# Performance work log

Hardware: AMD Instinct MI355X
Metric: run time of the kernel (lower is better)

Reference implementation:

```python
import jax, jax.numpy as jnp
import numpy as np

B, H, W, DIM, HEADS = 4, 32, 32, 768, 12
HD = DIM // HEADS


def setup_inputs() -> dict:
    key = jax.random.key(0)
    ks = jax.random.split(key, 5)
    return {
        "x": jax.random.normal(ks[0], (B, H, W, DIM), jnp.float32),
        "qkv_w": jax.random.normal(ks[1], (3 * DIM, DIM), jnp.float32) * 0.02,
        "qkv_b": jnp.zeros((3 * DIM,), jnp.float32),
        "proj_w": jax.random.normal(ks[2], (DIM, DIM), jnp.float32) * 0.02,
        "proj_b": jnp.zeros((DIM,), jnp.float32),
        "rel_pos_h": jax.random.normal(ks[3], (2 * H - 1, HD), jnp.float32) * 0.02,
        "rel_pos_w": jax.random.normal(ks[4], (2 * W - 1, HD), jnp.float32) * 0.02,
    }


def reference(x, qkv_w, qkv_b, proj_w, proj_b, rel_pos_h, rel_pos_w):
    b, h, w, dim = x.shape
    heads = HEADS
    hd = dim // heads
    n = h * w
    scale = hd ** -0.5

    xf = x.reshape(b, n, dim)
    qkv = xf @ qkv_w.T + qkv_b                          # [b, n, 3*dim]
    qkv = qkv.reshape(b, n, 3, heads, hd)
    qkv = jnp.transpose(qkv, (2, 0, 3, 1, 4)).reshape(3, b * heads, n, hd)
    q, k, v = qkv[0], qkv[1], qkv[2]                    # [b*heads, n, hd]

    # decomposed relative position bias (q_size == k_size, no interpolation)
    idx_h = jnp.arange(h)[:, None] - jnp.arange(h)[None, :] + (h - 1)
    idx_w = jnp.arange(w)[:, None] - jnp.arange(w)[None, :] + (w - 1)
    Rh = rel_pos_h[idx_h]                               # [h, h, hd]
    Rw = rel_pos_w[idx_w]                               # [w, w, hd]
    r_q = q.reshape(b * heads, h, w, hd)
    rel_h = jnp.einsum('bhwc,hkc->bhwk', r_q, Rh)       # [bH, h, w, h]
    rel_w = jnp.einsum('bhwc,wkc->bhwk', r_q, Rw)       # [bH, h, w, w]
    bias = (rel_h[:, :, :, :, None] + rel_w[:, :, :, None, :]).reshape(b * heads, n, n)

    attn = jax.nn.softmax(jnp.einsum('bnd,bmd->bnm', q * scale, k) + bias, axis=-1)
    out = jnp.einsum('bnm,bmd->bnd', attn, v)           # [b*heads, n, hd]
    out = out.reshape(b, heads, n, hd).transpose(0, 2, 1, 3).reshape(b, n, dim)
    out = out @ proj_w.T + proj_b
    return out.reshape(b, h, w, dim)
```

## Files before the change

kernel.cpp:

```cpp
#include <hip/hip_runtime.h>

#define DEV_INLINE static __device__ __forceinline__

typedef __attribute__((ext_vector_type(8))) short bf16x8;
typedef __attribute__((ext_vector_type(4))) float f32x4;
typedef __attribute__((ext_vector_type(16))) float f32x16;

DEV_INLINE unsigned short f2bf(float f) {
  union { float f; unsigned int u; } v; v.f = f;
  unsigned int u = v.u;
  u += 0x7FFFu + ((u >> 16) & 1u);
  return (unsigned short)(u >> 16);
}
DEV_INLINE float bf2f(unsigned short h) {
  union { unsigned int u; float f; } v; v.u = ((unsigned int)h) << 16; return v.f;
}

__global__ __launch_bounds__(256) void cvt_f32_bf16(const float* __restrict__ in,
                                                    unsigned short* __restrict__ out, int n4) {
  int i = blockIdx.x * 256 + threadIdx.x;
  if (i >= n4) return;
  float4 v = reinterpret_cast<const float4*>(in)[i];
  ushort4 o;
  o.x = f2bf(v.x); o.y = f2bf(v.y); o.z = f2bf(v.z); o.w = f2bf(v.w);
  reinterpret_cast<ushort4*>(out)[i] = o;
}

template <int MODE>
__global__ __launch_bounds__(256) void gemm_bf16(const unsigned short* __restrict__ A,
                                                 const unsigned short* __restrict__ Bw,
                                                 const float* __restrict__ bias,
                                                 float* __restrict__ outF,
                                                 unsigned short* __restrict__ qo,
                                                 unsigned short* __restrict__ ko,
                                                 unsigned short* __restrict__ vo) {
  __shared__ unsigned short As[2][128 * 32];
  __shared__ unsigned short Bs[2][128 * 32];

  const int tid = threadIdx.x;
  const int lane = tid & 63;
  const int wv = tid >> 6;
  const int wrow = (wv >> 1) * 64;
  const int wcol = (wv & 1) * 64;
  const int m0 = blockIdx.y * 128;
  const int n0 = blockIdx.x * 128;
  const int l15 = lane & 15;
  const int lg = lane >> 4;

  const int srow = lane >> 2;
  const int seg  = (lane & 3) ^ (srow & 3);

  f32x4 acc[4][4];
#pragma unroll
  for (int i = 0; i < 4; ++i)
#pragma unroll
    for (int j = 0; j < 4; ++j) acc[i][j] = (f32x4){0.f, 0.f, 0.f, 0.f};

#define GSTAGE(KT, B)                                                                        \
  do {                                                                                       \
    _Pragma("unroll") for (int pp = 0; pp < 2; ++pp) {                                       \
      int p = wv * 2 + pp;                                   \
      int row = p * 16 + srow;                                                               \
      const unsigned short* ga = &A[(m0 + row) * 768 + (KT) * 32 + seg * 8];                 \
      __builtin_amdgcn_global_load_lds(                                                      \
          (const __attribute__((address_space(1))) unsigned int*)ga,                         \
          (__attribute__((address_space(3))) unsigned int*)&As[B][p * 512], 16, 0, 0);       \
      const unsigned short* gb = &Bw[(n0 + row) * 768 + (KT) * 32 + seg * 8];                \
      __builtin_amdgcn_global_load_lds(                                                      \
          (const __attribute__((address_space(1))) unsigned int*)gb,                         \
          (__attribute__((address_space(3))) unsigned int*)&Bs[B][p * 512], 16, 0, 0);       \
    }                                                                                        \
  } while (0)

  GSTAGE(0, 0);

  for (int kt = 0; kt < 24; ++kt) {
    const int b = kt & 1;
    __syncthreads();
    if (kt < 23) GSTAGE(kt + 1, b ^ 1);

    const int soff = (lg ^ (l15 & 3)) * 8;
    bf16x8 aF[4], bF[4];
#pragma unroll
    for (int i = 0; i < 4; ++i)
      aF[i] = *reinterpret_cast<const bf16x8*>(&As[b][(wrow + i * 16 + l15) * 32 + soff]);
#pragma unroll
    for (int j = 0; j < 4; ++j)
      bF[j] = *reinterpret_cast<const bf16x8*>(&Bs[b][(wcol + j * 16 + l15) * 32 + soff]);
#pragma unroll
    for (int i = 0; i < 4; ++i)
#pragma unroll
      for (int j = 0; j < 4; ++j)
        acc[i][j] = __builtin_amdgcn_mfma_f32_16x16x32_bf16(aF[i], bF[j], acc[i][j], 0, 0, 0);
  }
#undef GSTAGE

#pragma unroll
  for (int i = 0; i < 4; ++i) {
#pragma unroll
    for (int j = 0; j < 4; ++j) {
#pragma unroll
      for (int r = 0; r < 4; ++r) {
        int row = m0 + wrow + i * 16 + (lane >> 4) * 4 + r;
        int col = n0 + wcol + j * 16 + l15;
        float val = acc[i][j][r] + bias[col];
        if (MODE == 0) {
          int t = col / 768;
          int rem = col - t * 768;
          int head = rem >> 6;
          int c = rem & 63;
          int bb = row >> 10;
          int n = row & 1023;
          if (t == 0) val *= 1.44269504f;
          if (t == 1) val *= 0.125f;
          unsigned short* dst = (t == 0) ? qo : (t == 1) ? ko : vo;
          dst[((bb * 12 + head) * 1024 + n) * 64 + c] = f2bf(val);
        } else {
          outF[row * 768 + col] = val;
        }
      }
    }
  }
}

__global__ __launch_bounds__(256) void vtrans(const unsigned short* __restrict__ vb,
                                              unsigned short* __restrict__ vt) {
  __shared__ unsigned short t[64][72];
  const int n0 = blockIdx.x * 64;
  const int bh = blockIdx.y;
  const int tid = threadIdx.x;
#pragma unroll
  for (int i = 0; i < 4; ++i) {
    int s = tid + i * 256;
    int row = s >> 4, c4 = (s & 15) * 4;
    *reinterpret_cast<ushort4*>(&t[row][c4]) =
        *reinterpret_cast<const ushort4*>(&vb[(bh * 1024 + n0 + row) * 64 + c4]);
  }
  __syncthreads();
#pragma unroll
  for (int i = 0; i < 4; ++i) {
    int s = tid + i * 256;
    int d = s >> 4, n4 = (s & 15) * 4;
    ushort4 o;
    o.x = t[n4 + 0][d]; o.y = t[n4 + 1][d]; o.z = t[n4 + 2][d]; o.w = t[n4 + 3][d];
    *reinterpret_cast<ushort4*>(&vt[(bh * 64 + d) * 1024 + n0 + n4]) = o;
  }
}

DEV_INLINE f32x4 mfma16(bf16x8 a, bf16x8 b, f32x4 c) {
  return __builtin_amdgcn_mfma_f32_16x16x32_bf16(a, b, c, 0, 0, 0);
}

__global__ __launch_bounds__(64) void rel_mfma16(const unsigned short* __restrict__ q,
                                                 const float* __restrict__ rph,
                                                 const float* __restrict__ rpw,
                                                 unsigned short* __restrict__ relwb,
                                                 float* __restrict__ relh) {
  __shared__ unsigned short qs[32 * 72];
  __shared__ unsigned short rhh[32 * 72], rhl[32 * 72];
  __shared__ unsigned short rwh[64 * 72], rwl[64 * 72];
  __shared__ float relh_s[32 * 36];
  __shared__ unsigned short relw_s[32 * 40];

  const int lane = threadIdx.x;
  const int l15 = lane & 15;
  const int lg = lane >> 4;
  const int qh = blockIdx.x;
  const int bh = blockIdx.y;

#pragma unroll
  for (int it = 0; it < 4; ++it) {
    int s = lane + it * 64;
    int row = s >> 3, ch = s & 7;
    *reinterpret_cast<int4*>(&qs[row * 72 + ch * 8]) =
        *reinterpret_cast<const int4*>(&q[(bh * 1024 + qh * 32 + row) * 64 + ch * 8]);
  }
#pragma unroll
  for (int it = 0; it < 8; ++it) {
    int s = lane + it * 64;
    int row = s >> 4, c4 = (s & 15) * 4;
    float4 v = *reinterpret_cast<const float4*>(&rph[(qh + row) * 64 + c4]);
    ushort4 h, l;
    h.x = f2bf(v.x); l.x = f2bf(v.x - bf2f(h.x));
    h.y = f2bf(v.y); l.y = f2bf(v.y - bf2f(h.y));
    h.z = f2bf(v.z); l.z = f2bf(v.z - bf2f(h.z));
    h.w = f2bf(v.w); l.w = f2bf(v.w - bf2f(h.w));
    *reinterpret_cast<ushort4*>(&rhh[row * 72 + c4]) = h;
    *reinterpret_cast<ushort4*>(&rhl[row * 72 + c4]) = l;
  }
#pragma unroll
  for (int it = 0; it < 16; ++it) {
    int s = lane + it * 64;
    int row = s >> 4, c4 = (s & 15) * 4;
    float4 v = (float4){0.f, 0.f, 0.f, 0.f};
    if (row < 63) v = *reinterpret_cast<const float4*>(&rpw[row * 64 + c4]);
    ushort4 h, l;
    h.x = f2bf(v.x); l.x = f2bf(v.x - bf2f(h.x));
    h.y = f2bf(v.y); l.y = f2bf(v.y - bf2f(h.y));
    h.z = f2bf(v.z); l.z = f2bf(v.z - bf2f(h.z));
    h.w = f2bf(v.w); l.w = f2bf(v.w - bf2f(h.w));
    *reinterpret_cast<ushort4*>(&rwh[row * 72 + c4]) = h;
    *reinterpret_cast<ushort4*>(&rwl[row * 72 + c4]) = l;
  }
  __syncthreads();

  const int k0 = lg * 8, k1 = 32 + lg * 8;
  bf16x8 fq[2][2], fhh[2][2], fhl[2][2], fwh[4][2], fwl[4][2];
#pragma unroll
  for (int t = 0; t < 2; ++t) {
    fq[t][0]  = *reinterpret_cast<const bf16x8*>(&qs[(t * 16 + l15) * 72 + k0]);
    fq[t][1]  = *reinterpret_cast<const bf16x8*>(&qs[(t * 16 + l15) * 72 + k1]);
    fhh[t][0] = *reinterpret_cast<const bf16x8*>(&rhh[(t * 16 + l15) * 72 + k0]);
    fhh[t][1] = *reinterpret_cast<const bf16x8*>(&rhh[(t * 16 + l15) * 72 + k1]);
    fhl[t][0] = *reinterpret_cast<const bf16x8*>(&rhl[(t * 16 + l15) * 72 + k0]);
    fhl[t][1] = *reinterpret_cast<const bf16x8*>(&rhl[(t * 16 + l15) * 72 + k1]);
  }
#pragma unroll
  for (int t = 0; t < 4; ++t) {
    fwh[t][0] = *reinterpret_cast<const bf16x8*>(&rwh[(t * 16 + l15) * 72 + k0]);
    fwh[t][1] = *reinterpret_cast<const bf16x8*>(&rwh[(t * 16 + l15) * 72 + k1]);
    fwl[t][0] = *reinterpret_cast<const bf16x8*>(&rwl[(t * 16 + l15) * 72 + k0]);
    fwl[t][1] = *reinterpret_cast<const bf16x8*>(&rwl[(t * 16 + l15) * 72 + k1]);
  }

  f32x4 ah[2][2];
#pragma unroll
  for (int i = 0; i < 2; ++i)
#pragma unroll
    for (int jj = 0; jj < 2; ++jj) {
      f32x4 a = (f32x4){0.f, 0.f, 0.f, 0.f};
      a = mfma16(fhh[i][0], fq[jj][0], a);
      a = mfma16(fhh[i][1], fq[jj][1], a);
      a = mfma16(fhl[i][0], fq[jj][0], a);
      a = mfma16(fhl[i][1], fq[jj][1], a);
      ah[i][jj] = a;
    }
  f32x4 aw[2][4];
#pragma unroll
  for (int i = 0; i < 2; ++i)
#pragma unroll
    for (int jj = 0; jj < 4; ++jj) {
      f32x4 a = (f32x4){0.f, 0.f, 0.f, 0.f};
      a = mfma16(fq[i][0], fwh[jj][0], a);
      a = mfma16(fq[i][1], fwh[jj][1], a);
      a = mfma16(fq[i][0], fwl[jj][0], a);
      a = mfma16(fq[i][1], fwl[jj][1], a);
      aw[i][jj] = a;
    }

#pragma unroll
  for (int i = 0; i < 2; ++i)
#pragma unroll
    for (int jj = 0; jj < 2; ++jj)
#pragma unroll
      for (int r = 0; r < 4; ++r) {
        int t = i * 16 + lg * 4 + r;
        int qw = jj * 16 + l15;
        relh_s[qw * 36 + 31 - t] = ah[i][jj][r];
      }
#pragma unroll
  for (int i = 0; i < 2; ++i)
#pragma unroll
    for (int jj = 0; jj < 4; ++jj)
#pragma unroll
      for (int r = 0; r < 4; ++r) {
        int qw = i * 16 + lg * 4 + r;
        int d = jj * 16 + l15;
        int kw = qw + 31 - d;
        if (kw >= 0 && kw < 32) relw_s[qw * 40 + kw] = f2bf(aw[i][jj][r]);
      }
  __syncthreads();

#pragma unroll
  for (int it = 0; it < 4; ++it) {
    int s = lane + it * 64;
    int row = s >> 3, c4 = (s & 7) * 4;
    *reinterpret_cast<float4*>(&relh[(bh * 1024 + qh * 32 + row) * 32 + c4]) =
        *reinterpret_cast<const float4*>(&relh_s[row * 36 + c4]);
  }
#pragma unroll
  for (int it = 0; it < 2; ++it) {
    int s = lane + it * 64;
    int row = s >> 2, ch = s & 3;
    *reinterpret_cast<int4*>(&relwb[(bh * 1024 + qh * 32 + row) * 32 + ch * 8]) =
        *reinterpret_cast<const int4*>(&relw_s[row * 40 + ch * 8]);
  }
}

DEV_INLINE f32x16 mfma32(bf16x8 a, bf16x8 b, f32x16 c) {
  return __builtin_amdgcn_mfma_f32_32x32x16_bf16(a, b, c, 0, 0, 0);
}

DEV_INLINE bf16x8 make_pa(const float* p) {
  unsigned int W0, W1, W2, W3;
  asm("v_cvt_pk_bf16_f32 %0, %1, %2" : "=v"(W0) : "v"(p[0]), "v"(p[1]));
  asm("v_cvt_pk_bf16_f32 %0, %1, %2" : "=v"(W1) : "v"(p[2]), "v"(p[3]));
  asm("v_cvt_pk_bf16_f32 %0, %1, %2" : "=v"(W2) : "v"(p[4]), "v"(p[5]));
  asm("v_cvt_pk_bf16_f32 %0, %1, %2" : "=v"(W3) : "v"(p[6]), "v"(p[7]));
  asm("v_permlane32_swap_b32 %0, %1" : "+v"(W0), "+v"(W2));
  asm("v_permlane32_swap_b32 %0, %1" : "+v"(W1), "+v"(W3));
  union { unsigned int w[4]; bf16x8 v; } u;
  u.w[0] = W0; u.w[1] = W1; u.w[2] = W2; u.w[3] = W3;
  return u.v;
}

__global__ __launch_bounds__(128) void attn2(const unsigned short* __restrict__ kg,
                                             const unsigned short* __restrict__ vtg,
                                             const unsigned short* __restrict__ qg,
                                             const unsigned short* __restrict__ relwb,
                                             const float* __restrict__ relh,
                                             unsigned short* __restrict__ ao) {
  __shared__ unsigned short k_lin[2][64 * 64];
  __shared__ unsigned short v_lin[2][64 * 64];

  const int tid = threadIdx.x;
  const int lane = tid & 63;
  const int wv = tid >> 6;
  const int l31 = lane & 31;
  const int hi = lane >> 5;

  const int bid = blockIdx.x;
  const int swz = (bid & 7) * 96 + (bid >> 3);
  const int bh = swz >> 4;
  const int qt = swz & 15;
  const int q0 = qt * 64 + wv * 32;

  bf16x8 qf[6];
  {
    const unsigned short* qrow = &qg[(bh * 1024 + q0 + l31) * 64 + hi * 8];
#pragma unroll
    for (int c = 0; c < 4; ++c)
      qf[c] = *reinterpret_cast<const bf16x8*>(&qrow[c * 16]);
    const unsigned short* wrow = &relwb[(bh * 1024 + q0 + l31) * 32 + hi * 8];
    qf[4] = *reinterpret_cast<const bf16x8*>(&wrow[0]);
    qf[5] = *reinterpret_cast<const bf16x8*>(&wrow[16]);
  }

  bf16x8 ohf0, ohf1;
  {
    int t0 = l31 - 8 * hi;
    int t1 = l31 - 16 - 8 * hi;
    union { unsigned int w[4]; bf16x8 v; } u0, u1;
#pragma unroll
    for (int w = 0; w < 4; ++w) {
      u0.w[w] = (t0 >= 0 && (t0 >> 1) == w) ? ((t0 & 1) ? 0x3F800000u : 0x3F80u) : 0u;
      u1.w[w] = (t1 >= 0 && (t1 >> 1) == w) ? ((t1 & 1) ? 0x3F800000u : 0x3F80u) : 0u;
    }
    ohf0 = u0.v; ohf1 = u1.v;
  }

  f32x16 O0, O1;
#pragma unroll
  for (int r = 0; r < 16; ++r) { O0[r] = 0.f; O1[r] = 0.f; }
  float m_r = -3.0e38f, l_r = 0.f;

  const int srow = lane >> 3;
  const int scb = (lane & 7) ^ srow;
  const int rsw = l31 & 7;

#define STAGE(KT, B)                                                                       \
  do {                                                                                     \
    _Pragma("unroll") for (int pp = 0; pp < 4; ++pp) {                                     \
      int p = wv * 4 + pp;                                                                 \
      int row = p * 8 + srow;                                                              \
      const unsigned short* gk = &kg[(bh * 1024 + (KT) * 64 + row) * 64 + scb * 8];        \
      __builtin_amdgcn_global_load_lds(                                                    \
          (const __attribute__((address_space(1))) unsigned int*)gk,                       \
          (__attribute__((address_space(3))) unsigned int*)&k_lin[B][p * 512], 16, 0, 0);  \
      const unsigned short* gv = &vtg[(bh * 64 + row) * 1024 + (KT) * 64 + scb * 8];       \
      __builtin_amdgcn_global_load_lds(                                                    \
          (const __attribute__((address_space(1))) unsigned int*)gv,                       \
          (__attribute__((address_space(3))) unsigned int*)&v_lin[B][p * 512], 16, 0, 0);  \
    }                                                                                      \
  } while (0)

  STAGE(0, 0);

  const float* rhrow = &relh[(bh * 1024 + q0 + l31) * 32];
  float2 bhv = *reinterpret_cast<const float2*>(&rhrow[0]);

  for (int kt = 0; kt < 16; ++kt) {
    const int b = kt & 1;
    __syncthreads();
    if (kt < 15) STAGE(kt + 1, b ^ 1);

    float2 bhv_next = bhv;
    if (kt < 15) bhv_next = *reinterpret_cast<const float2*>(&rhrow[2 * (kt + 1)]);
    float bh0 = bhv.x, bh1 = bhv.y;

    f32x16 s0, s1;
#pragma unroll
    for (int r = 0; r < 16; ++r) { s0[r] = 0.f; s1[r] = 0.f; }
    {
      const unsigned short* kb0 = &k_lin[b][l31 * 64];
      const unsigned short* kb1 = &k_lin[b][(32 + l31) * 64];
      __builtin_amdgcn_s_setprio(1);
#pragma unroll
      for (int c = 0; c < 4; ++c) {
        int cb = ((2 * c + hi) ^ rsw) * 8;
        s0 = mfma32(*reinterpret_cast<const bf16x8*>(&kb0[cb]), qf[c], s0);
        s1 = mfma32(*reinterpret_cast<const bf16x8*>(&kb1[cb]), qf[c], s1);
      }
      s0 = mfma32(ohf0, qf[4], s0);
      s0 = mfma32(ohf1, qf[5], s0);
      s1 = mfma32(ohf0, qf[4], s1);
      s1 = mfma32(ohf1, qf[5], s1);
      __builtin_amdgcn_s_setprio(0);
    }

    float pm0 = s0[0], pm1 = s1[0];
#pragma unroll
    for (int r = 1; r < 16; ++r) { pm0 = fmaxf(pm0, s0[r]); pm1 = fmaxf(pm1, s1[r]); }
    float pmax = fmaxf(pm0 + bh0, pm1 + bh1);
    pmax = fmaxf(pmax, __shfl_xor(pmax, 32));

    if (!__all(pmax <= m_r + 11.5f)) {
      float mnew = fmaxf(m_r, pmax);
      float corr = __builtin_amdgcn_exp2f(m_r - mnew);
      m_r = mnew;
      l_r *= corr;
#pragma unroll
      for (int r = 0; r < 16; ++r) {
        int cr = ((r & 3) + 8 * (r >> 2) + 4 * hi) << 2;
        float c2 = __int_as_float(__builtin_amdgcn_ds_bpermute(cr, __float_as_int(corr)));
        O0[r] *= c2;
        O1[r] *= c2;
      }
    }

    float mb0 = m_r - bh0, mb1 = m_r - bh1;
    float p0[16], p1[16];
    float ps = 0.f;
#pragma unroll
    for (int r = 0; r < 16; ++r) { p0[r] = __builtin_amdgcn_exp2f(s0[r] - mb0); ps += p0[r]; }
#pragma unroll
    for (int r = 0; r < 16; ++r) { p1[r] = __builtin_amdgcn_exp2f(s1[r] - mb1); ps += p1[r]; }
    ps += __shfl_xor(ps, 32);
    l_r += ps;

    bf16x8 pa0 = make_pa(p0 + 0);
    bf16x8 pa1 = make_pa(p0 + 8);
    bf16x8 pa2 = make_pa(p1 + 0);
    bf16x8 pa3 = make_pa(p1 + 8);

    const unsigned short* vb0 = &v_lin[b][l31 * 64];
    const unsigned short* vb1 = &v_lin[b][(32 + l31) * 64];
    __builtin_amdgcn_s_setprio(1);
#pragma unroll
    for (int c = 0; c < 4; ++c) {
      bf16x8 pac = (c == 0) ? pa0 : (c == 1) ? pa1 : (c == 2) ? pa2 : pa3;
      int cb = ((2 * c + hi) ^ rsw) * 8;
      O0 = mfma32(pac, *reinterpret_cast<const bf16x8*>(&vb0[cb]), O0);
      O1 = mfma32(pac, *reinterpret_cast<const bf16x8*>(&vb1[cb]), O1);
    }
    __builtin_amdgcn_s_setprio(0);

    bhv = bhv_next;
  }
#undef STAGE

  float invl = 1.f / l_r;
  const int bb = bh / 12, head = bh % 12;
#pragma unroll
  for (int r = 0; r < 16; ++r) {
    int crow = (r & 3) + 8 * (r >> 2) + 4 * hi;
    float il = __int_as_float(__builtin_amdgcn_ds_bpermute(crow << 2, __float_as_int(invl)));
    int n = q0 + crow;
    unsigned short* dst = &ao[(bb * 1024 + n) * 768 + head * 64];
    dst[l31] = f2bf(O0[r] * il);
    dst[32 + l31] = f2bf(O1[r] * il);
  }
}

extern "C" void kernel_launch(void* const* d_in, const int* in_sizes, int n_in,
                              void* d_out, int out_size, void* d_ws, size_t ws_size,
                              hipStream_t stream) {
  const float* x      = (const float*)d_in[0];
  const float* qkv_w  = (const float*)d_in[1];
  const float* qkv_b  = (const float*)d_in[2];
  const float* proj_w = (const float*)d_in[3];
  const float* proj_b = (const float*)d_in[4];
  const float* rph    = (const float*)d_in[5];
  const float* rpw    = (const float*)d_in[6];
  float* out = (float*)d_out;

  char* ws = (char*)d_ws;
  unsigned short* xb    = (unsigned short*)(ws);
  float*          relh  = (float*)(ws);
  unsigned short* wqkv  = (unsigned short*)(ws + 6291456);
  unsigned short* wproj = (unsigned short*)(ws + 9830400);
  unsigned short* qb    = (unsigned short*)(ws + 11010048);
  unsigned short* kb    = (unsigned short*)(ws + 17301504);
  unsigned short* vb    = (unsigned short*)(ws + 23592960);
  unsigned short* ao    = (unsigned short*)(ws + 23592960);
  unsigned short* vt    = (unsigned short*)(ws + 29884416);
  unsigned short* relwb = (unsigned short*)(ws + 36175872);

  cvt_f32_bf16<<<3072, 256, 0, stream>>>(x, xb, 786432);
  cvt_f32_bf16<<<1728, 256, 0, stream>>>(qkv_w, wqkv, 442368);
  cvt_f32_bf16<<<576, 256, 0, stream>>>(proj_w, wproj, 147456);

  gemm_bf16<0><<<dim3(18, 32), 256, 0, stream>>>(xb, wqkv, qkv_b, nullptr, qb, kb, vb);
  vtrans<<<dim3(16, 48), 256, 0, stream>>>(vb, vt);
  rel_mfma16<<<dim3(32, 48), 64, 0, stream>>>(qb, rph, rpw, relwb, relh);
  attn2<<<768, 128, 0, stream>>>(kb, vt, qb, relwb, relh, ao);
  gemm_bf16<1><<<dim3(6, 32), 256, 0, stream>>>(ao, wproj, proj_b, out, nullptr, nullptr, nullptr);
}
```

Measured before the change: 126.0 us.

## Triple-buffer LDS staging in GEMM and attention with explicit vmcnt waits

Both the projection GEMM and the attention kernel move from double to triple buffering of LDS tiles, issuing loads two stages ahead. The full __syncthreads is replaced by a partial s_waitcnt vmcnt on outstanding loads followed by s_barrier, so global loads can overlap more compute. The attention kernel also preloads the whole rel_h row into 32 registers instead of prefetching two values per iteration. The cost is more LDS per block, which may reduce occupancy, plus higher register pressure, and the hand-counted vmcnt values must match the actual number of loads in flight.

Result: slower. 128.8 us (+2.3%).

```diff
diff --git a/kernel.cpp b/kernel.cpp
--- a/kernel.cpp
+++ b/kernel.cpp
@@ -34,8 +34,8 @@
                                                  unsigned short* __restrict__ qo,
                                                  unsigned short* __restrict__ ko,
                                                  unsigned short* __restrict__ vo) {
-  __shared__ unsigned short As[2][128 * 32];
-  __shared__ unsigned short Bs[2][128 * 32];
+  __shared__ unsigned short As[3][128 * 32];
+  __shared__ unsigned short Bs[3][128 * 32];
 
   const int tid = threadIdx.x;
   const int lane = tid & 63;
@@ -73,13 +73,19 @@
   } while (0)
 
   GSTAGE(0, 0);
-
+  GSTAGE(1, 1);
+
+  const int soff = (lg ^ (l15 & 3)) * 8;
+
+#pragma unroll
   for (int kt = 0; kt < 24; ++kt) {
-    const int b = kt & 1;
-    __syncthreads();
-    if (kt < 23) GSTAGE(kt + 1, b ^ 1);
-
-    const int soff = (lg ^ (l15 & 3)) * 8;
+    const int b = kt % 3;
+    if (kt < 23) asm volatile("s_waitcnt vmcnt(4)" ::: "memory");
+    else         asm volatile("s_waitcnt vmcnt(0)" ::: "memory");
+    __builtin_amdgcn_s_barrier();
+    asm volatile("" ::: "memory");
+    if (kt < 22) GSTAGE(kt + 2, (kt + 2) % 3);
+
     bf16x8 aF[4], bF[4];
 #pragma unroll
     for (int i = 0; i < 4; ++i)
@@ -310,8 +316,8 @@
                                              const unsigned short* __restrict__ relwb,
                                              const float* __restrict__ relh,
                                              unsigned short* __restrict__ ao) {
-  __shared__ unsigned short k_lin[2][64 * 64];
-  __shared__ unsigned short v_lin[2][64 * 64];
+  __shared__ unsigned short k_lin[3][64 * 64];
+  __shared__ unsigned short v_lin[3][64 * 64];
 
   const int tid = threadIdx.x;
   const int lane = tid & 63;
@@ -347,6 +353,17 @@
       u1.w[w] = (t1 >= 0 && (t1 >> 1) == w) ? ((t1 & 1) ? 0x3F800000u : 0x3F80u) : 0u;
     }
     ohf0 = u0.v; ohf1 = u1.v;
+  }
+
+  float bhr[32];
+  {
+    const float* rhrow = &relh[(bh * 1024 + q0 + l31) * 32];
+#pragma unroll
+    for (int i = 0; i < 8; ++i) {
+      float4 t4 = *reinterpret_cast<const float4*>(&rhrow[i * 4]);
+      bhr[i * 4 + 0] = t4.x; bhr[i * 4 + 1] = t4.y;
+      bhr[i * 4 + 2] = t4.z; bhr[i * 4 + 3] = t4.w;
+    }
   }
 
   f32x16 O0, O1;
@@ -375,18 +392,18 @@
   } while (0)
 
   STAGE(0, 0);
-
-  const float* rhrow = &relh[(bh * 1024 + q0 + l31) * 32];
-  float2 bhv = *reinterpret_cast<const float2*>(&rhrow[0]);
-
+  STAGE(1, 1);
+
+#pragma unroll
   for (int kt = 0; kt < 16; ++kt) {
-    const int b = kt & 1;
-    __syncthreads();
-    if (kt < 15) STAGE(kt + 1, b ^ 1);
-
-    float2 bhv_next = bhv;
-    if (kt < 15) bhv_next = *reinterpret_cast<const float2*>(&rhrow[2 * (kt + 1)]);
-    float bh0 = bhv.x, bh1 = bhv.y;
+    const int b = kt % 3;
+    if (kt < 15) asm volatile("s_waitcnt vmcnt(8)" ::: "memory");
+    else         asm volatile("s_waitcnt vmcnt(0)" ::: "memory");
+    __builtin_amdgcn_s_barrier();
+    asm volatile("" ::: "memory");
+    if (kt < 14) STAGE(kt + 2, (kt + 2) % 3);
+
+    float bh0 = bhr[2 * kt], bh1 = bhr[2 * kt + 1];
 
     f32x16 s0, s1;
 #pragma unroll
@@ -454,8 +471,6 @@
       O1 = mfma32(pac, *reinterpret_cast<const bf16x8*>(&vb1[cb]), O1);
     }
     __builtin_amdgcn_s_setprio(0);
-
-    bhv = bhv_next;
   }
 #undef STAGE
 
```
